# Performance work log

Hardware: AMD Instinct MI355X
Metric: run time of the kernel (lower is better)

The kernel has to match this reference:

```python
import jax, jax.numpy as jnp
import numpy as np

N_ING, N_TASTE, D, E = 50000, 20000, 128, 600000


def setup_inputs() -> dict:
    key = jax.random.key(0)
    ks = jax.random.split(key, 13)
    s = 1.0 / np.sqrt(D)
    src = jax.random.randint(ks[2], (E,), 0, N_ING)
    dst = jax.random.randint(ks[3], (E,), 0, N_TASTE)
    return {
        "x_ing": jax.random.normal(ks[0], (N_ING, D), jnp.float32),
        "x_taste": jax.random.normal(ks[1], (N_TASTE, D), jnp.float32),
        "edge_index": jnp.stack([src, dst]),  # [2, E], row0=src(ingredient), row1=dst(taste)
        "W_ing": (jax.random.normal(ks[4], (D, D), jnp.float32) * s),
        "b_ing": jnp.zeros((D,), jnp.float32),
        "W_taste": (jax.random.normal(ks[5], (D, D), jnp.float32) * s),
        "b_taste": jnp.zeros((D,), jnp.float32),
        "a_src": (jax.random.normal(ks[6], (D,), jnp.float32) * s),
        "a_dst": (jax.random.normal(ks[7], (D,), jnp.float32) * s),
        "Wk": (jax.random.normal(ks[8], (D, D), jnp.float32) * s),
        "bk": jnp.zeros((D,), jnp.float32),
        "q": (jax.random.normal(ks[9], (D,), jnp.float32) * s),
    }


def reference(x_ing, x_taste, edge_index, W_ing, b_ing, W_taste, b_taste,
              a_src, a_dst, Wk, bk, q):
    # Input DictDropout(0.4) treated as identity (eval mode) for determinism.
    Nt = x_taste.shape[0]
    src, dst = edge_index[0], edge_index[1]

    # Per-node-type projections (HANConv.proj), heads=1 so head dim == D
    h_src = x_ing @ W_ing + b_ing      # [Ni, D]
    h_dst = x_taste @ W_taste + b_taste  # [Nt, D]

    # GAT-style additive attention logits
    al_src = h_src @ a_src  # [Ni]
    al_dst = h_dst @ a_dst  # [Nt]
    alpha = jax.nn.leaky_relu(al_src[src] + al_dst[dst], negative_slope=0.2)  # [E]

    # scatter-softmax over destination nodes
    amax = jax.ops.segment_max(alpha, dst, num_segments=Nt)        # [Nt]
    e = jnp.exp(alpha - amax[dst])                                  # [E]
    denom = jax.ops.segment_sum(e, dst, num_segments=Nt)           # [Nt]
    attn = e / jnp.maximum(denom[dst], 1e-16)                       # [E]

    # weighted scatter-add aggregation + ReLU (as in HANConv per edge type)
    msgs = h_src[src] * attn[:, None]                               # [E, D]
    out = jax.ops.segment_sum(msgs, dst, num_segments=Nt)          # [Nt, D]
    out = jax.nn.relu(out)

    # semantic attention across relation types (single relation -> beta == 1)
    score = jnp.sum(jnp.tanh(out @ Wk + bk).mean(axis=0) * q)       # scalar
    beta = jax.nn.softmax(score[None])[0]
    out = beta * out

    # TasteGNN applies GELU (torch default: exact erf form)
    return jax.nn.gelu(out, approximate=False)
```

## Files before the change

### kernel.cpp

```cpp
#include <hip/hip_runtime.h>
#include <hip/hip_bf16.h>

#define D 128
#define NT 20000
#define CHUNK_SHIFT 15
#define CHUNK (1 << CHUNK_SHIFT)
#define MAXNB 19

using bf16x8 = __attribute__((ext_vector_type(8))) short;
using f32x4  = __attribute__((ext_vector_type(4))) float;

__device__ __forceinline__ ushort bf16bits(float f) {
    return __hip_bfloat16_raw(__float2bfloat16(f)).x;
}
__device__ __forceinline__ uint pack2(float lo, float hi) {
    return ((uint)bf16bits(hi) << 16) | (uint)bf16bits(lo);
}

__global__ __launch_bounds__(256)
void front_kernel(const float* __restrict__ x, const float* __restrict__ W_ing,
                  const float* __restrict__ b, const float* __restrict__ avec,
                  const float* __restrict__ W_taste, const float* __restrict__ b_taste,
                  const float* __restrict__ a_dst,
                  ushort* __restrict__ h16, int nrows, int GB,
                  const float* __restrict__ x_taste,
                  int nt, float* __restrict__ al_src, float* __restrict__ al_dst,
                  const int* __restrict__ dstv, int E, int NB,
                  int* __restrict__ hists, unsigned char* __restrict__ rank,
                  int* __restrict__ total) {
    __shared__ __align__(16) union {
        struct { ushort Xs[128 * 64]; ushort Ws[128 * 64]; } stage;
        ushort Os[128 * 128];
        uint hist8[NT / 4];
        float v[128];
    } sm;
    int t = threadIdx.x;

    if (blockIdx.x < (uint)NB) {
        int c = blockIdx.x;
        for (int i = t; i < NT / 4; i += 256) sm.hist8[i] = 0;
        __syncthreads();
        int beg = c << CHUNK_SHIFT;
        int end = beg + CHUNK; if (end > E) end = E;
        for (int i0 = beg + t; i0 < end; i0 += 256 * 8) {
            int idx[8], dv[8]; uint rv[8];
            #pragma unroll
            for (int k = 0; k < 8; ++k) {
                idx[k] = i0 + k * 256;
                dv[k] = (idx[k] < end) ? dstv[idx[k]] : -1;
            }
            #pragma unroll
            for (int k = 0; k < 8; ++k)
                rv[k] = (dv[k] >= 0)
                    ? atomicAdd(&sm.hist8[dv[k] >> 2], 1u << ((dv[k] & 3) * 8)) : 0u;
            #pragma unroll
            for (int k = 0; k < 8; ++k)
                if (dv[k] >= 0)
                    rank[idx[k]] = (unsigned char)((rv[k] >> ((dv[k] & 3) * 8)) & 0xffu);
        }
        __syncthreads();
        int* hb = hists + (size_t)c * nt;
        for (int d2 = t; d2 < nt; d2 += 256)
            hb[d2] = (int)((sm.hist8[d2 >> 2] >> ((d2 & 3) * 8)) & 0xffu);
        return;
    }
    if (blockIdx.x >= (uint)(NB + GB)) {
        int rb = blockIdx.x - NB - GB;
        int lane = t & 63;
        if (rb == 0 && t == 0) *total = 0;
        if (t < 128) {
            const float* wr = W_taste + (size_t)t * D;
            float sv = 0.f;
            for (int d2 = 0; d2 < D; ++d2) sv += wr[d2] * a_dst[d2];
            sm.v[t] = sv;
        }
        float c1 = b_taste[2 * lane] * a_dst[2 * lane]
                 + b_taste[2 * lane + 1] * a_dst[2 * lane + 1];
        #pragma unroll
        for (int off = 32; off; off >>= 1) c1 += __shfl_xor(c1, off, 64);
        __syncthreads();
        int wave = rb * 4 + (t >> 6);
        float2 uv = ((const float2*)sm.v)[lane];
        for (int r = wave; r < nt; r += 2048) {
            float2 xv = ((const float2*)(x_taste + (size_t)r * D))[lane];
            float p = xv.x * uv.x + xv.y * uv.y;
            #pragma unroll
            for (int off = 32; off; off >>= 1) p += __shfl_xor(p, off, 64);
            if (lane == 0) al_dst[r] = p + c1;
        }
        return;
    }

    int row0 = (blockIdx.x - NB) * 128;
    int l = t & 63, w = t >> 6;
    int lr = l & 15, lq = l >> 4;
    f32x4 acc[2][8];
    #pragma unroll
    for (int i = 0; i < 2; ++i)
        #pragma unroll
        for (int j = 0; j < 8; ++j) acc[i][j] = f32x4{0.f, 0.f, 0.f, 0.f};

    int rowA0 = w * 32 + lr;
    int rowA1 = rowA0 + 16;
    int sw = lr & 7;
    int r = t >> 1;
    int kh = (t & 1) * 32;
    bool valid = (row0 + r) < nrows;
    int kk = t >> 2;
    int seg = t & 3;

    #pragma unroll
    for (int h = 0; h < 2; ++h) {
        int k0 = h * 64;
        {
            const float* xp = x + (size_t)(row0 + r) * D + k0 + kh;
            int base_us = r * 64;
            #pragma unroll
            for (int j = 0; j < 4; ++j) {
                int c16 = (kh >> 3) + j;
                int off = base_us + ((c16 ^ (r & 7)) << 3);
                float4 a = valid ? *(const float4*)(xp + j * 8)     : make_float4(0.f, 0.f, 0.f, 0.f);
                float4 c = valid ? *(const float4*)(xp + j * 8 + 4) : make_float4(0.f, 0.f, 0.f, 0.f);
                uint4 pk;
                pk.x = pack2(a.x, a.y); pk.y = pack2(a.z, a.w);
                pk.z = pack2(c.x, c.y); pk.w = pack2(c.z, c.w);
                *(uint4*)&sm.stage.Xs[off] = pk;
            }
            const float* wrow = W_ing + (size_t)(k0 + kk) * D + seg * 32;
            int ccb = kk >> 3, klo = kk & 7;
            #pragma unroll
            for (int j = 0; j < 8; ++j) {
                float4 wv = *(const float4*)(wrow + j * 4);
                int n0 = seg * 32 + j * 4;
                sm.stage.Ws[(n0    ) * 64 + ((ccb ^ ((n0    ) & 7)) << 3) + klo] = bf16bits(wv.x);
                sm.stage.Ws[(n0 + 1) * 64 + ((ccb ^ ((n0 + 1) & 7)) << 3) + klo] = bf16bits(wv.y);
                sm.stage.Ws[(n0 + 2) * 64 + ((ccb ^ ((n0 + 2) & 7)) << 3) + klo] = bf16bits(wv.z);
                sm.stage.Ws[(n0 + 3) * 64 + ((ccb ^ ((n0 + 3) & 7)) << 3) + klo] = bf16bits(wv.w);
            }
        }
        __syncthreads();
        #pragma unroll
        for (int s = 0; s < 2; ++s) {
            int c16 = s * 4 + lq;
            bf16x8 A0 = *(const bf16x8*)&sm.stage.Xs[rowA0 * 64 + ((c16 ^ sw) << 3)];
            bf16x8 A1 = *(const bf16x8*)&sm.stage.Xs[rowA1 * 64 + ((c16 ^ sw) << 3)];
            #pragma unroll
            for (int ct = 0; ct < 8; ++ct) {
                int rn = ct * 16 + lr;
                bf16x8 B = *(const bf16x8*)&sm.stage.Ws[rn * 64 + ((c16 ^ sw) << 3)];
                acc[0][ct] = __builtin_amdgcn_mfma_f32_16x16x32_bf16(A0, B, acc[0][ct], 0, 0, 0);
                acc[1][ct] = __builtin_amdgcn_mfma_f32_16x16x32_bf16(A1, B, acc[1][ct], 0, 0, 0);
            }
        }
        __syncthreads();
    }

    float bv[8], av[8];
    #pragma unroll
    for (int ct = 0; ct < 8; ++ct) { bv[ct] = b[ct * 16 + lr]; av[ct] = avec[ct * 16 + lr]; }
    float pc = 0.f;
    #pragma unroll
    for (int ct = 0; ct < 8; ++ct) pc = fmaf(bv[ct], av[ct], pc);
    pc += __shfl_xor(pc, 1, 64); pc += __shfl_xor(pc, 2, 64);
    pc += __shfl_xor(pc, 4, 64); pc += __shfl_xor(pc, 8, 64);
    float c0 = pc;
    #pragma unroll
    for (int rt = 0; rt < 2; ++rt) {
        #pragma unroll
        for (int rr = 0; rr < 4; ++rr) {
            int rl = w * 32 + rt * 16 + lq * 4 + rr;
            int rsw = rl & 7;
            float p = 0.f;
            #pragma unroll
            for (int ct = 0; ct < 8; ++ct) {
                float hv = acc[rt][ct][rr] + bv[ct];
                p = fmaf(hv, av[ct], p);
                int cc = ct * 16 + lr;
                sm.Os[rl * 128 + (((cc >> 3) ^ rsw) << 3) + (cc & 7)] = bf16bits(hv);
            }
            p += __shfl_xor(p, 1, 64); p += __shfl_xor(p, 2, 64);
            p += __shfl_xor(p, 4, 64); p += __shfl_xor(p, 8, 64);
            int gr = row0 + rl;
            if (lr == 0 && gr < nrows) al_src[gr] = p + c0;
        }
    }
    __syncthreads();
    #pragma unroll
    for (int i = t; i < 2048; i += 256) {
        int rl = i >> 4, cs = i & 15;
        int gr = row0 + rl;
        if (gr < nrows)
            *(uint4*)&h16[(size_t)gr * D + cs * 8] =
                *(const uint4*)&sm.Os[rl * 128 + ((cs ^ (rl & 7)) << 3)];
    }
}

__global__ __launch_bounds__(256)
void alloc2_kernel(int* __restrict__ hists, int nt, int NB,
                   int* __restrict__ offs, int* __restrict__ count,
                   int* __restrict__ total) {
    int gid = blockIdx.x * blockDim.x + threadIdx.x;
    int lane = threadIdx.x & 63;
    int vals[MAXNB];
    if (gid < nt) {
        #pragma unroll
        for (int b = 0; b < MAXNB; ++b)
            vals[b] = (b < NB) ? hists[(size_t)b * nt + gid] : 0;
    }
    int run = 0;
    if (gid < nt) {
        #pragma unroll
        for (int b = 0; b < MAXNB; ++b) {
            int vv = vals[b]; vals[b] = run; run += vv;
        }
        count[gid] = run;
    }
    int s = run;
    #pragma unroll
    for (int off = 1; off < 64; off <<= 1) {
        int t2 = __shfl_up(s, off, 64);
        if (lane >= off) s += t2;
    }
    int wavesum = __shfl(s, 63, 64);
    int base = 0;
    if (lane == 63) base = atomicAdd(total, wavesum);
    base = __shfl(base, 63, 64);
    if (gid < nt) {
        int o = base + s - run;
        offs[gid] = o;
        #pragma unroll
        for (int b = 0; b < MAXNB; ++b)
            if (b < NB) hists[(size_t)b * nt + gid] = vals[b] + o;
    }
}

__global__ __launch_bounds__(256)
void scatter_kernel(const int* __restrict__ srcv, const int* __restrict__ dstv,
                    const unsigned char* __restrict__ rank, int E, int nt,
                    const int* __restrict__ hists, uint* __restrict__ es) {
    int tbase = blockIdx.x * blockDim.x + threadIdx.x;
    int stride = gridDim.x * blockDim.x;
    for (int i0 = tbase; i0 < E; i0 += stride * 8) {
        int idx[8], sv[8], dv[8], rv[8], ov[8];
        #pragma unroll
        for (int k = 0; k < 8; ++k) {
            idx[k] = i0 + k * stride;
            bool val = idx[k] < E;
            sv[k] = val ? srcv[idx[k]] : 0;
            dv[k] = val ? dstv[idx[k]] : 0;
            rv[k] = val ? (int)rank[idx[k]] : 0;
        }
        #pragma unroll
        for (int k = 0; k < 8; ++k) {
            int bb = idx[k] >> CHUNK_SHIFT;
            ov[k] = (idx[k] < E) ? hists[(size_t)bb * nt + dv[k]] : 0;
        }
        #pragma unroll
        for (int k = 0; k < 8; ++k)
            if (idx[k] < E) es[ov[k] + rv[k]] = (uint)sv[k];
    }
}

__global__ __launch_bounds__(256)
void agg_kernel(const ushort* __restrict__ h16, const int* __restrict__ offs,
                const int* __restrict__ count, const uint* __restrict__ es,
                const float* __restrict__ al_src, const float* __restrict__ al_dst,
                int nt, float* __restrict__ outp) {
    int lane = threadIdx.x & 63;
    int n = blockIdx.x * (blockDim.x >> 6) + (threadIdx.x >> 6);
    if (n >= nt) return;
    int beg = offs[n], cnt = count[n];
    float acc0 = 0.f, acc1 = 0.f;
    if (cnt > 0) {
        float ald = al_dst[n];
        uint s0 = 0, s1 = 0;
        float a0 = -1e30f, a1 = -1e30f;
        if (lane < cnt) {
            s0 = es[beg + lane];
            float t = al_src[s0] + ald; a0 = t > 0.f ? t : 0.2f * t;
        }
        if (64 + lane < cnt) {
            s1 = es[beg + 64 + lane];
            float t = al_src[s1] + ald; a1 = t > 0.f ? t : 0.2f * t;
        }
        float m = fmaxf(a0, a1);
        for (int i = 128 + lane; i < cnt; i += 64) {
            uint s = es[beg + i];
            float t = al_src[s] + ald; t = t > 0.f ? t : 0.2f * t;
            m = fmaxf(m, t);
        }
        #pragma unroll
        for (int off = 32; off; off >>= 1) m = fmaxf(m, __shfl_xor(m, off, 64));

        float w0 = (lane < cnt) ? __expf(a0 - m) : 0.f;
        float w1 = (64 + lane < cnt) ? __expf(a1 - m) : 0.f;
        float ssum = w0 + w1;
        for (int i = 128 + lane; i < cnt; i += 64) {
            uint s = es[beg + i];
            float t = al_src[s] + ald; t = t > 0.f ? t : 0.2f * t;
            ssum += __expf(t - m);
        }
        #pragma unroll
        for (int off = 32; off; off >>= 1) ssum += __shfl_xor(ssum, off, 64);
        float inv = 1.f / fmaxf(ssum, 1e-16f);

        for (int base = 0; base < cnt; base += 64) {
            uint pkl;
            if (base == 0)       pkl = (s0 << 16) | ((__float_as_uint(w0) + 0x8000u) >> 16);
            else if (base == 64) pkl = (s1 << 16) | ((__float_as_uint(w1) + 0x8000u) >> 16);
            else {
                pkl = 0;
                if (base + lane < cnt) {
                    uint s = es[beg + base + lane];
                    float t = al_src[s] + ald; t = t > 0.f ? t : 0.2f * t;
                    float wv = __expf(t - m);
                    pkl = (s << 16) | ((__float_as_uint(wv) + 0x8000u) >> 16);
                }
            }
            if (base + lane >= cnt) pkl = 0;
            int k = cnt - base; if (k > 64) k = 64;
            int kpad = (k + 15) & ~15;
            for (int i = 0; i < kpad; i += 16) {
                uint pk[16], hv[16];
                #pragma unroll
                for (int j = 0; j < 16; ++j) pk[j] = __shfl(pkl, i + j, 64);
                #pragma unroll
                for (int j = 0; j < 16; ++j) {
                    uint s2 = pk[j] >> 16;
                    hv[j] = ((const uint*)(h16 + (size_t)s2 * D))[lane];
                }
                #pragma unroll
                for (int j = 0; j < 16; ++j) {
                    float w  = __uint_as_float(pk[j] << 16);
                    float lo = __uint_as_float((hv[j] & 0xffffu) << 16);
                    float hi = __uint_as_float(hv[j] & 0xffff0000u);
                    acc0 = fmaf(w, lo, acc0);
                    acc1 = fmaf(w, hi, acc1);
                }
            }
        }
        acc0 *= inv; acc1 *= inv;
    }
    float o0 = acc0 > 0.f ? acc0 : 0.f;
    float o1 = acc1 > 0.f ? acc1 : 0.f;
    o0 = 0.5f * o0 * (1.f + erff(o0 * 0.70710678118654752f));
    o1 = 0.5f * o1 * (1.f + erff(o1 * 0.70710678118654752f));
    *(float2*)(outp + (size_t)n * D + 2 * lane) = make_float2(o0, o1);
}

extern "C" void kernel_launch(void* const* d_in, const int* in_sizes, int n_in,
                              void* d_out, int out_size, void* d_ws, size_t ws_size,
                              hipStream_t stream) {
    const float* x_ing   = (const float*)d_in[0];
    const float* x_taste = (const float*)d_in[1];
    const int*   edge    = (const int*)d_in[2];
    const float* W_ing   = (const float*)d_in[3];
    const float* b_ing   = (const float*)d_in[4];
    const float* W_taste = (const float*)d_in[5];
    const float* b_taste = (const float*)d_in[6];
    const float* a_src   = (const float*)d_in[7];
    const float* a_dst   = (const float*)d_in[8];
    float* outp = (float*)d_out;

    int Ni = in_sizes[0] / D;
    int Nt = in_sizes[1] / D;
    int E  = in_sizes[2] / 2;
    const int* srcv = edge;
    const int* dstv = edge + E;

    char* ws = (char*)d_ws;
    size_t off = 0;
    auto alloc = [&](size_t bytes) { void* p = ws + off; off += (bytes + 255) & ~(size_t)255; return p; };
    ushort* h16   = (ushort*)alloc((size_t)Ni * D * 2);
    float* al_src = (float*)alloc((size_t)Ni * 4);
    float* al_dst = (float*)alloc((size_t)Nt * 4);
    int* count    = (int*)alloc((size_t)Nt * 4);
    int* offs     = (int*)alloc((size_t)Nt * 4);
    unsigned char* rank = (unsigned char*)alloc((size_t)E);
    int* total    = (int*)alloc(4);
    uint* es      = (uint*)alloc((size_t)E * 4);
    int NB = (E + CHUNK - 1) >> CHUNK_SHIFT;
    int* hists    = (int*)alloc((size_t)NB * Nt * 4);

    int GB = (Ni + 127) / 128;
    front_kernel<<<NB + GB + 512, 256, 0, stream>>>(x_ing, W_ing, b_ing, a_src,
                                                    W_taste, b_taste, a_dst,
                                                    h16, Ni, GB,
                                                    x_taste, Nt, al_src, al_dst,
                                                    dstv, E, NB, hists, rank, total);
    alloc2_kernel<<<(Nt + 255) / 256, 256, 0, stream>>>(hists, Nt, NB, offs, count, total);
    int sb = (E + 256 * 8 - 1) / (256 * 8);
    scatter_kernel<<<sb, 256, 0, stream>>>(srcv, dstv, rank, E, Nt, hists, es);
    agg_kernel<<<(Nt + 3) / 4, 256, 0, stream>>>(h16, offs, count, es, al_src, al_dst, Nt, outp);
}
```

Measured before the change: 74.34 us.

## Build per-chunk CSR in front kernel and drop global alloc/scatter passes

Each edge-histogram block now does a local exclusive scan of its 16-bit per-destination counts and scatters source ids straight into a chunk-local edge array. The separate global prefix-sum and scatter kernels go away, removing two launches and the global rank and offset traffic. In exchange, the aggregation kernel must rebuild each node's edge positions across up to 19 chunk segments and map every edge index through a per-lane segment search. This adds ALU work and makes edge reads non-contiguous across chunks.

```diff
diff --git a/kernel.cpp b/kernel.cpp
--- a/kernel.cpp
+++ b/kernel.cpp
@@ -6,6 +6,7 @@
 #define CHUNK_SHIFT 15
 #define CHUNK (1 << CHUNK_SHIFT)
 #define MAXNB 19
+#define NTP 20002
 
 using bf16x8 = __attribute__((ext_vector_type(8))) short;
 using f32x4  = __attribute__((ext_vector_type(4))) float;
@@ -25,49 +26,96 @@
                   ushort* __restrict__ h16, int nrows, int GB,
                   const float* __restrict__ x_taste,
                   int nt, float* __restrict__ al_src, float* __restrict__ al_dst,
-                  const int* __restrict__ dstv, int E, int NB,
-                  int* __restrict__ hists, unsigned char* __restrict__ rank,
-                  int* __restrict__ total) {
+                  const int* __restrict__ srcv, const int* __restrict__ dstv,
+                  int E, int NB,
+                  ushort* __restrict__ hists16, uint* __restrict__ es) {
     __shared__ __align__(16) union {
         struct { ushort Xs[128 * 64]; ushort Ws[128 * 64]; } stage;
         ushort Os[128 * 128];
-        uint hist8[NT / 4];
+        uint ofs[NT / 2];
         float v[128];
     } sm;
+    __shared__ int wsum[4];
     int t = threadIdx.x;
 
     if (blockIdx.x < (uint)NB) {
         int c = blockIdx.x;
-        for (int i = t; i < NT / 4; i += 256) sm.hist8[i] = 0;
-        __syncthreads();
-        int beg = c << CHUNK_SHIFT;
-        int end = beg + CHUNK; if (end > E) end = E;
-        for (int i0 = beg + t; i0 < end; i0 += 256 * 8) {
-            int idx[8], dv[8]; uint rv[8];
+        int cbase = c << CHUNK_SHIFT;
+        int cend = cbase + CHUNK; if (cend > E) cend = E;
+        int csize = cend - cbase;
+        for (int i = t; i < NT / 2; i += 256) sm.ofs[i] = 0;
+        __syncthreads();
+        for (int i0 = cbase + t; i0 < cend; i0 += 256 * 8) {
+            int dv[8];
+            #pragma unroll
+            for (int k = 0; k < 8; ++k) {
+                int idx = i0 + k * 256;
+                dv[k] = (idx < cend) ? dstv[idx] : -1;
+            }
+            #pragma unroll
+            for (int k = 0; k < 8; ++k)
+                if (dv[k] >= 0) atomicAdd(&sm.ofs[dv[k] >> 1], 1u << ((dv[k] & 1) * 16));
+        }
+        __syncthreads();
+        int lane = t & 63, wv = t >> 6;
+        int s0 = t * 40;
+        int tot = 0;
+        if (t < 250) {
+            for (int w2 = 0; w2 < 40; ++w2) {
+                uint u = sm.ofs[s0 + w2];
+                tot += (int)(u & 0xffffu) + (int)(u >> 16);
+            }
+        }
+        int incl = tot;
+        #pragma unroll
+        for (int off = 1; off < 64; off <<= 1) {
+            int xx = __shfl_up(incl, off, 64);
+            if (lane >= off) incl += xx;
+        }
+        if (lane == 63) wsum[wv] = incl;
+        __syncthreads();
+        int wbase = 0;
+        for (int j = 0; j < 4; ++j) if (j < wv) wbase += wsum[j];
+        int base = wbase + (incl - tot);
+        if (t < 250) {
+            int running = base;
+            for (int w2 = 0; w2 < 40; ++w2) {
+                uint u = sm.ofs[s0 + w2];
+                uint lo = u & 0xffffu, hi = u >> 16;
+                sm.ofs[s0 + w2] = (uint)running | ((uint)(running + (int)lo) << 16);
+                running += (int)(lo + hi);
+            }
+        }
+        __syncthreads();
+        ushort* hb = hists16 + (size_t)c * NTP;
+        for (int i = t; i < NT / 2; i += 256) ((uint*)hb)[i] = sm.ofs[i];
+        if (t == 0) hb[NT] = (ushort)csize;
+        __syncthreads();
+        for (int i0 = cbase + t; i0 < cend; i0 += 256 * 8) {
+            int idx[8], dv[8], sv[8]; uint rv[8];
             #pragma unroll
             for (int k = 0; k < 8; ++k) {
                 idx[k] = i0 + k * 256;
-                dv[k] = (idx[k] < end) ? dstv[idx[k]] : -1;
+                bool val = idx[k] < cend;
+                dv[k] = val ? dstv[idx[k]] : -1;
+                sv[k] = val ? srcv[idx[k]] : 0;
             }
             #pragma unroll
             for (int k = 0; k < 8; ++k)
                 rv[k] = (dv[k] >= 0)
-                    ? atomicAdd(&sm.hist8[dv[k] >> 2], 1u << ((dv[k] & 3) * 8)) : 0u;
+                    ? atomicAdd(&sm.ofs[dv[k] >> 1], 1u << ((dv[k] & 1) * 16)) : 0u;
             #pragma unroll
             for (int k = 0; k < 8; ++k)
-                if (dv[k] >= 0)
-                    rank[idx[k]] = (unsigned char)((rv[k] >> ((dv[k] & 3) * 8)) & 0xffu);
-        }
-        __syncthreads();
-        int* hb = hists + (size_t)c * nt;
-        for (int d2 = t; d2 < nt; d2 += 256)
-            hb[d2] = (int)((sm.hist8[d2 >> 2] >> ((d2 & 3) * 8)) & 0xffu);
+                if (dv[k] >= 0) {
+                    int pos = (int)((rv[k] >> ((dv[k] & 1) * 16)) & 0xffffu);
+                    es[cbase + pos] = (uint)sv[k];
+                }
+        }
         return;
     }
     if (blockIdx.x >= (uint)(NB + GB)) {
         int rb = blockIdx.x - NB - GB;
         int lane = t & 63;
-        if (rb == 0 && t == 0) *total = 0;
         if (t < 128) {
             const float* wr = W_taste + (size_t)t * D;
             float sv = 0.f;
@@ -130,12 +178,12 @@
             int ccb = kk >> 3, klo = kk & 7;
             #pragma unroll
             for (int j = 0; j < 8; ++j) {
-                float4 wv = *(const float4*)(wrow + j * 4);
+                float4 wv4 = *(const float4*)(wrow + j * 4);
                 int n0 = seg * 32 + j * 4;
-                sm.stage.Ws[(n0    ) * 64 + ((ccb ^ ((n0    ) & 7)) << 3) + klo] = bf16bits(wv.x);
-                sm.stage.Ws[(n0 + 1) * 64 + ((ccb ^ ((n0 + 1) & 7)) << 3) + klo] = bf16bits(wv.y);
-                sm.stage.Ws[(n0 + 2) * 64 + ((ccb ^ ((n0 + 2) & 7)) << 3) + klo] = bf16bits(wv.z);
-                sm.stage.Ws[(n0 + 3) * 64 + ((ccb ^ ((n0 + 3) & 7)) << 3) + klo] = bf16bits(wv.w);
+                sm.stage.Ws[(n0    ) * 64 + ((ccb ^ ((n0    ) & 7)) << 3) + klo] = bf16bits(wv4.x);
+                sm.stage.Ws[(n0 + 1) * 64 + ((ccb ^ ((n0 + 1) & 7)) << 3) + klo] = bf16bits(wv4.y);
+                sm.stage.Ws[(n0 + 2) * 64 + ((ccb ^ ((n0 + 2) & 7)) << 3) + klo] = bf16bits(wv4.z);
+                sm.stage.Ws[(n0 + 3) * 64 + ((ccb ^ ((n0 + 3) & 7)) << 3) + klo] = bf16bits(wv4.w);
             }
         }
         __syncthreads();
@@ -196,96 +244,60 @@
 }
 
 __global__ __launch_bounds__(256)
-void alloc2_kernel(int* __restrict__ hists, int nt, int NB,
-                   int* __restrict__ offs, int* __restrict__ count,
-                   int* __restrict__ total) {
-    int gid = blockIdx.x * blockDim.x + threadIdx.x;
-    int lane = threadIdx.x & 63;
-    int vals[MAXNB];
-    if (gid < nt) {
-        #pragma unroll
-        for (int b = 0; b < MAXNB; ++b)
-            vals[b] = (b < NB) ? hists[(size_t)b * nt + gid] : 0;
-    }
-    int run = 0;
-    if (gid < nt) {
-        #pragma unroll
-        for (int b = 0; b < MAXNB; ++b) {
-            int vv = vals[b]; vals[b] = run; run += vv;
-        }
-        count[gid] = run;
-    }
-    int s = run;
-    #pragma unroll
-    for (int off = 1; off < 64; off <<= 1) {
-        int t2 = __shfl_up(s, off, 64);
-        if (lane >= off) s += t2;
-    }
-    int wavesum = __shfl(s, 63, 64);
-    int base = 0;
-    if (lane == 63) base = atomicAdd(total, wavesum);
-    base = __shfl(base, 63, 64);
-    if (gid < nt) {
-        int o = base + s - run;
-        offs[gid] = o;
-        #pragma unroll
-        for (int b = 0; b < MAXNB; ++b)
-            if (b < NB) hists[(size_t)b * nt + gid] = vals[b] + o;
-    }
-}
-
-__global__ __launch_bounds__(256)
-void scatter_kernel(const int* __restrict__ srcv, const int* __restrict__ dstv,
-                    const unsigned char* __restrict__ rank, int E, int nt,
-                    const int* __restrict__ hists, uint* __restrict__ es) {
-    int tbase = blockIdx.x * blockDim.x + threadIdx.x;
-    int stride = gridDim.x * blockDim.x;
-    for (int i0 = tbase; i0 < E; i0 += stride * 8) {
-        int idx[8], sv[8], dv[8], rv[8], ov[8];
-        #pragma unroll
-        for (int k = 0; k < 8; ++k) {
-            idx[k] = i0 + k * stride;
-            bool val = idx[k] < E;
-            sv[k] = val ? srcv[idx[k]] : 0;
-            dv[k] = val ? dstv[idx[k]] : 0;
-            rv[k] = val ? (int)rank[idx[k]] : 0;
-        }
-        #pragma unroll
-        for (int k = 0; k < 8; ++k) {
-            int bb = idx[k] >> CHUNK_SHIFT;
-            ov[k] = (idx[k] < E) ? hists[(size_t)bb * nt + dv[k]] : 0;
-        }
-        #pragma unroll
-        for (int k = 0; k < 8; ++k)
-            if (idx[k] < E) es[ov[k] + rv[k]] = (uint)sv[k];
-    }
-}
-
-__global__ __launch_bounds__(256)
-void agg_kernel(const ushort* __restrict__ h16, const int* __restrict__ offs,
-                const int* __restrict__ count, const uint* __restrict__ es,
+void agg_kernel(const ushort* __restrict__ h16, const ushort* __restrict__ hists16,
+                const uint* __restrict__ es,
                 const float* __restrict__ al_src, const float* __restrict__ al_dst,
-                int nt, float* __restrict__ outp) {
+                int nt, int NB, float* __restrict__ outp) {
     int lane = threadIdx.x & 63;
     int n = blockIdx.x * (blockDim.x >> 6) + (threadIdx.x >> 6);
     if (n >= nt) return;
-    int beg = offs[n], cnt = count[n];
+
+    int o0 = 0, cntc = 0;
+    if (lane < NB) {
+        const ushort* hb = hists16 + (size_t)lane * NTP;
+        o0 = hb[n];
+        cntc = (int)hb[n + 1] - o0;
+    }
+    int incl = cntc;
+    #pragma unroll
+    for (int off = 1; off < 64; off <<= 1) {
+        int xx = __shfl_up(incl, off, 64);
+        if (lane >= off) incl += xx;
+    }
+    int cnt = __shfl(incl, NB - 1, 64);
+    int segO[MAXNB], segE[MAXNB];
+    #pragma unroll
+    for (int cc = 0; cc < MAXNB; ++cc) {
+        segO[cc] = __shfl(o0, cc, 64);
+        segE[cc] = __shfl(incl, cc, 64);
+    }
+    auto esIdx = [&](int e) {
+        int res = 0, st = 0;
+        #pragma unroll
+        for (int cc = 0; cc < MAXNB; ++cc) {
+            int en = segE[cc];
+            if (e >= st && e < en) res = cc * CHUNK + segO[cc] + (e - st);
+            st = en;
+        }
+        return res;
+    };
+
     float acc0 = 0.f, acc1 = 0.f;
     if (cnt > 0) {
         float ald = al_dst[n];
         uint s0 = 0, s1 = 0;
         float a0 = -1e30f, a1 = -1e30f;
         if (lane < cnt) {
-            s0 = es[beg + lane];
+            s0 = es[esIdx(lane)];
             float t = al_src[s0] + ald; a0 = t > 0.f ? t : 0.2f * t;
         }
         if (64 + lane < cnt) {
-            s1 = es[beg + 64 + lane];
+            s1 = es[esIdx(64 + lane)];
             float t = al_src[s1] + ald; a1 = t > 0.f ? t : 0.2f * t;
         }
         float m = fmaxf(a0, a1);
         for (int i = 128 + lane; i < cnt; i += 64) {
-            uint s = es[beg + i];
+            uint s = es[esIdx(i)];
             float t = al_src[s] + ald; t = t > 0.f ? t : 0.2f * t;
             m = fmaxf(m, t);
         }
@@ -296,7 +308,7 @@
         float w1 = (64 + lane < cnt) ? __expf(a1 - m) : 0.f;
         float ssum = w0 + w1;
         for (int i = 128 + lane; i < cnt; i += 64) {
-            uint s = es[beg + i];
+            uint s = es[esIdx(i)];
             float t = al_src[s] + ald; t = t > 0.f ? t : 0.2f * t;
             ssum += __expf(t - m);
         }
@@ -311,7 +323,7 @@
             else {
                 pkl = 0;
                 if (base + lane < cnt) {
-                    uint s = es[beg + base + lane];
+                    uint s = es[esIdx(base + lane)];
                     float t = al_src[s] + ald; t = t > 0.f ? t : 0.2f * t;
                     float wv = __expf(t - m);
                     pkl = (s << 16) | ((__float_as_uint(wv) + 0x8000u) >> 16);
@@ -341,11 +353,11 @@
         }
         acc0 *= inv; acc1 *= inv;
     }
-    float o0 = acc0 > 0.f ? acc0 : 0.f;
-    float o1 = acc1 > 0.f ? acc1 : 0.f;
-    o0 = 0.5f * o0 * (1.f + erff(o0 * 0.70710678118654752f));
-    o1 = 0.5f * o1 * (1.f + erff(o1 * 0.70710678118654752f));
-    *(float2*)(outp + (size_t)n * D + 2 * lane) = make_float2(o0, o1);
+    float o0f = acc0 > 0.f ? acc0 : 0.f;
+    float o1f = acc1 > 0.f ? acc1 : 0.f;
+    o0f = 0.5f * o0f * (1.f + erff(o0f * 0.70710678118654752f));
+    o1f = 0.5f * o1f * (1.f + erff(o1f * 0.70710678118654752f));
+    *(float2*)(outp + (size_t)n * D + 2 * lane) = make_float2(o0f, o1f);
 }
 
 extern "C" void kernel_launch(void* const* d_in, const int* in_sizes, int n_in,
@@ -371,25 +383,19 @@
     char* ws = (char*)d_ws;
     size_t off = 0;
     auto alloc = [&](size_t bytes) { void* p = ws + off; off += (bytes + 255) & ~(size_t)255; return p; };
-    ushort* h16   = (ushort*)alloc((size_t)Ni * D * 2);
-    float* al_src = (float*)alloc((size_t)Ni * 4);
-    float* al_dst = (float*)alloc((size_t)Nt * 4);
-    int* count    = (int*)alloc((size_t)Nt * 4);
-    int* offs     = (int*)alloc((size_t)Nt * 4);
-    unsigned char* rank = (unsigned char*)alloc((size_t)E);
-    int* total    = (int*)alloc(4);
-    uint* es      = (uint*)alloc((size_t)E * 4);
+    ushort* h16     = (ushort*)alloc((size_t)Ni * D * 2);
+    float* al_src   = (float*)alloc((size_t)Ni * 4);
+    float* al_dst   = (float*)alloc((size_t)Nt * 4);
+    uint* es        = (uint*)alloc((size_t)(((size_t)MAXNB) << CHUNK_SHIFT) * 4);
+    ushort* hists16 = (ushort*)alloc((size_t)MAXNB * NTP * 2);
+
     int NB = (E + CHUNK - 1) >> CHUNK_SHIFT;
-    int* hists    = (int*)alloc((size_t)NB * Nt * 4);
-
     int GB = (Ni + 127) / 128;
     front_kernel<<<NB + GB + 512, 256, 0, stream>>>(x_ing, W_ing, b_ing, a_src,
                                                     W_taste, b_taste, a_dst,
                                                     h16, Ni, GB,
                                                     x_taste, Nt, al_src, al_dst,
-                                                    dstv, E, NB, hists, rank, total);
-    alloc2_kernel<<<(Nt + 255) / 256, 256, 0, stream>>>(hists, Nt, NB, offs, count, total);
-    int sb = (E + 256 * 8 - 1) / (256 * 8);
-    scatter_kernel<<<sb, 256, 0, stream>>>(srcv, dstv, rank, E, Nt, hists, es);
-    agg_kernel<<<(Nt + 3) / 4, 256, 0, stream>>>(h16, offs, count, es, al_src, al_dst, Nt, outp);
+                                                    srcv, dstv, E, NB, hists16, es);
+    agg_kernel<<<(Nt + 3) / 4, 256, 0, stream>>>(h16, hists16, es, al_src, al_dst,
+                                                 Nt, NB, outp);
 }
```

Measured after the change: 94.83 us. +27.6%, slower.
